# Kernel tuning notes

Measured on AMD Instinct MI355X. Metric: run time of the kernel, lower is better.

Reference implementation:

```python
import jax, jax.numpy as jnp
import numpy as np
import math

DIM = 1024
DIM_HEAD = 64
HEADS = 16
B, N = 2, 2048


def _layernorm(x, g, b, eps=1e-5):
    x32 = x.astype(jnp.float32)
    mu = jnp.mean(x32, axis=-1, keepdims=True)
    var = jnp.var(x32, axis=-1, keepdims=True)
    return ((x32 - mu) * jax.lax.rsqrt(var + eps) * g + b).astype(x.dtype)


def setup_inputs() -> dict:
    key = jax.random.key(0)
    ks = jax.random.split(key, 8)
    inner = DIM_HEAD * HEADS
    return {
        "x": jax.random.normal(ks[0], (B, N, DIM), dtype=jnp.float32),
        "w_q": jax.random.normal(ks[1], (inner, DIM), dtype=jnp.float32) * 0.02,
        "w_kv": jax.random.normal(ks[2], (2 * DIM_HEAD, DIM), dtype=jnp.float32) * 0.02,
        "w_out": jax.random.normal(ks[3], (DIM, inner), dtype=jnp.float32) * 0.02,
        "ln_g": jnp.ones((DIM,), dtype=jnp.float32),
        "ln_b": jnp.zeros((DIM,), dtype=jnp.float32),
        "lno_g": jnp.ones((DIM,), dtype=jnp.float32),
        "lno_b": jnp.zeros((DIM,), dtype=jnp.float32),
    }


def reference(x, w_q, w_kv, w_out, ln_g, ln_b, lno_g, lno_b):
    b, n, _ = x.shape
    scale = DIM_HEAD ** -0.5
    xn = _layernorm(x, ln_g, ln_b)
    q = jnp.einsum('bnc,ec->bne', xn, w_q)                 # [b, n, h*d]
    kv = jnp.einsum('bnc,ec->bne', xn, w_kv)               # [b, n, 2*d]
    k, v = jnp.split(kv, 2, axis=-1)                        # each [b, n, d]
    q = q.reshape(b, n, HEADS, DIM_HEAD).transpose(0, 2, 1, 3)  # [b, h, n, d]
    # faithful double scaling: q*scale then q,k each *sqrt(scale)
    sqs = math.sqrt(scale)
    q = q * (scale * sqs)
    k = k * sqs
    sim = jnp.einsum('bhid,bjd->bhij', q, k)                # [b, h, n, n]
    max_neg = -jnp.finfo(sim.dtype).max
    causal_mask = jnp.triu(jnp.ones((n, n), dtype=bool), k=1)
    sim = jnp.where(causal_mask, max_neg, sim)
    attn = jax.nn.softmax(sim.astype(jnp.float32), axis=-1).astype(sim.dtype)
    out = jnp.einsum('bhij,bjd->bhid', attn, v)             # [b, h, n, d]
    out = out.transpose(0, 2, 1, 3).reshape(b, n, HEADS * DIM_HEAD)
    out = jnp.einsum('bne,ce->bnc', out, w_out)             # [b, n, dim]
    return _layernorm(out, lno_g, lno_b)
```

## Files before the change

### kernel.cpp

```cpp
#include <hip/hip_runtime.h>
#include <hip/hip_bf16.h>
#include <stdint.h>

typedef unsigned short u16;
typedef __bf16 bf16x8 __attribute__((ext_vector_type(8)));
typedef float f32x4 __attribute__((ext_vector_type(4)));

#define MFMA16(a, b, c) __builtin_amdgcn_mfma_f32_16x16x32_bf16((a), (b), (c), 0, 0, 0)

#define BATCH 2
#define NSEQ 2048
#define DIMC 1024
#define NHEAD 16
#define DHEAD 64

__device__ __forceinline__ u16 f2bf(float f) {
  unsigned u = __float_as_uint(f);
  u += 0x7FFFu + ((u >> 16) & 1u);
  return (u16)(u >> 16);
}
__device__ __forceinline__ float bf2f(u16 h) {
  return __uint_as_float(((unsigned)h) << 16);
}
__device__ __forceinline__ void gload_lds16(const void* g, void* lds) {
  __builtin_amdgcn_global_load_lds((const __attribute__((address_space(1))) void*)g,
                                   (__attribute__((address_space(3))) void*)lds,
                                   16, 0, 0);
}
#define WAIT_VM(N) asm volatile("s_waitcnt vmcnt(" #N ")" ::: "memory")
#define BARRIER() __builtin_amdgcn_s_barrier()

__global__ __launch_bounds__(256) void cvt_f32_bf16(const float* __restrict__ in,
                                                    u16* __restrict__ out, int n) {
  int i = (blockIdx.x * 256 + threadIdx.x) * 4;
  if (i < n) {
    float4 v = *(const float4*)(in + i);
    ushort4 o;
    o.x = f2bf(v.x); o.y = f2bf(v.y); o.z = f2bf(v.z); o.w = f2bf(v.w);
    *(ushort4*)(out + i) = o;
  }
}

__global__ __launch_bounds__(256) void ln_f32_to_bf16(const float* __restrict__ X,
                                                      const float* __restrict__ G,
                                                      const float* __restrict__ Bv,
                                                      u16* __restrict__ Y) {
  const int row = blockIdx.x;
  const int tid = threadIdx.x;
  const float4 v = *(const float4*)(X + (size_t)row * DIMC + tid * 4);
  float s = v.x + v.y + v.z + v.w;
  float q = v.x * v.x + v.y * v.y + v.z * v.z + v.w * v.w;
#pragma unroll
  for (int d = 1; d < 64; d <<= 1) {
    s += __shfl_xor(s, d, 64);
    q += __shfl_xor(q, d, 64);
  }
  __shared__ float ps[4], pq[4];
  const int w = tid >> 6, l = tid & 63;
  if (l == 0) { ps[w] = s; pq[w] = q; }
  __syncthreads();
  s = ps[0] + ps[1] + ps[2] + ps[3];
  q = pq[0] + pq[1] + pq[2] + pq[3];
  const float mean = s * (1.f / DIMC);
  const float var = q * (1.f / DIMC) - mean * mean;
  const float rs = rsqrtf(var + 1e-5f);
  const float4 g = *(const float4*)(G + tid * 4);
  const float4 bb = *(const float4*)(Bv + tid * 4);
  ushort4 o;
  o.x = f2bf((v.x - mean) * rs * g.x + bb.x);
  o.y = f2bf((v.y - mean) * rs * g.y + bb.y);
  o.z = f2bf((v.z - mean) * rs * g.z + bb.z);
  o.w = f2bf((v.w - mean) * rs * g.w + bb.w);
  *(ushort4*)(Y + (size_t)row * DIMC + tid * 4) = o;
}

__global__ __launch_bounds__(256) void ln_bf16_to_f32(const u16* __restrict__ X,
                                                      const float* __restrict__ G,
                                                      const float* __restrict__ Bv,
                                                      float* __restrict__ Y) {
  const int row = blockIdx.x;
  const int tid = threadIdx.x;
  const ushort4 hv = *(const ushort4*)(X + (size_t)row * DIMC + tid * 4);
  float x0 = bf2f(hv.x), x1 = bf2f(hv.y), x2 = bf2f(hv.z), x3 = bf2f(hv.w);
  float s = x0 + x1 + x2 + x3;
  float q = x0 * x0 + x1 * x1 + x2 * x2 + x3 * x3;
#pragma unroll
  for (int d = 1; d < 64; d <<= 1) {
    s += __shfl_xor(s, d, 64);
    q += __shfl_xor(q, d, 64);
  }
  __shared__ float ps[4], pq[4];
  const int w = tid >> 6, l = tid & 63;
  if (l == 0) { ps[w] = s; pq[w] = q; }
  __syncthreads();
  s = ps[0] + ps[1] + ps[2] + ps[3];
  q = pq[0] + pq[1] + pq[2] + pq[3];
  const float mean = s * (1.f / DIMC);
  const float var = q * (1.f / DIMC) - mean * mean;
  const float rs = rsqrtf(var + 1e-5f);
  const float4 g = *(const float4*)(G + tid * 4);
  const float4 bb = *(const float4*)(Bv + tid * 4);
  float4 o;
  o.x = (x0 - mean) * rs * g.x + bb.x;
  o.y = (x1 - mean) * rs * g.y + bb.y;
  o.z = (x2 - mean) * rs * g.z + bb.z;
  o.w = (x3 - mean) * rs * g.w + bb.w;
  *(float4*)(Y + (size_t)row * DIMC + tid * 4) = o;
}

template <int MODE>
__global__ __launch_bounds__(512, 4) void gemm_bt(const u16* __restrict__ A,
                                                  const u16* __restrict__ Bw,
                                                  u16* __restrict__ out0,
                                                  u16* __restrict__ out1,
                                                  u16* __restrict__ out2,
                                                  int M, int N, int K, float scale0) {
  const int tid = threadIdx.x;
  const int w = tid >> 6, l = tid & 63;
  const int wr = w >> 2, wc = w & 3;
  const int lr = l & 15, lg = l >> 4;

  const int nwgx = gridDim.x;
  const int nwg = nwgx * gridDim.y;
  int flat = blockIdx.x + nwgx * blockIdx.y;
  flat = (flat & 7) * (nwg >> 3) + (flat >> 3);
  const int m0 = (flat / nwgx) * 128, n0 = (flat % nwgx) * 128;

  __shared__ u16 As[2][128 * 64];
  __shared__ u16 Bs[2][128 * 64];

  f32x4 acc[4][2] = {};

  auto STAGE = [&](int buf, int kt) {
#pragma unroll
    for (int r = 0; r < 2; ++r) {
      const int c = w * 2 + r;
      const int lo = c * 1024 + l * 16;
      const int row = lo >> 7;
      const int cl = (lo & 127) ^ ((row & 7) << 4);
      gload_lds16((const char*)A + ((size_t)(m0 + row) * K + kt * 64) * 2 + cl,
                  (char*)As[buf] + c * 1024);
      gload_lds16((const char*)Bw + ((size_t)(n0 + row) * K + kt * 64) * 2 + cl,
                  (char*)Bs[buf] + c * 1024);
    }
  };

  const int nk = K >> 6;
  STAGE(0, 0);
  STAGE(1, 1);
  int cur = 0;
  for (int kt = 0; kt < nk; ++kt) {
    if (kt + 1 < nk) { WAIT_VM(4); } else { WAIT_VM(0); }
    BARRIER();
    const char* as = (const char*)As[cur];
    const char* bs = (const char*)Bs[cur];
#pragma unroll
    for (int ks = 0; ks < 2; ++ks) {
      bf16x8 af[4], bfr[2];
#pragma unroll
      for (int mi = 0; mi < 4; ++mi) {
        const int row = wr * 64 + mi * 16 + lr;
        af[mi] = *(const bf16x8*)(as + row * 128 + ((ks * 64 + lg * 16) ^ ((row & 7) << 4)));
      }
#pragma unroll
      for (int ni = 0; ni < 2; ++ni) {
        const int row = wc * 32 + ni * 16 + lr;
        bfr[ni] = *(const bf16x8*)(bs + row * 128 + ((ks * 64 + lg * 16) ^ ((row & 7) << 4)));
      }
      __builtin_amdgcn_s_setprio(1);
#pragma unroll
      for (int mi = 0; mi < 4; ++mi)
#pragma unroll
        for (int ni = 0; ni < 2; ++ni)
          acc[mi][ni] = MFMA16(af[mi], bfr[ni], acc[mi][ni]);
      __builtin_amdgcn_s_setprio(0);
    }
    BARRIER();
    if (kt + 2 < nk) STAGE(cur, kt + 2);
    cur ^= 1;
  }

  if constexpr (MODE == 0) {
#pragma unroll
    for (int mi = 0; mi < 4; ++mi)
#pragma unroll
      for (int ni = 0; ni < 2; ++ni)
#pragma unroll
        for (int r = 0; r < 4; ++r) {
          const int row = m0 + wr * 64 + mi * 16 + lg * 4 + r;
          const int col = n0 + wc * 32 + ni * 16 + lr;
          out0[(size_t)row * N + col] = f2bf(acc[mi][ni][r] * scale0);
        }
  } else {
    const float sqs = 0.35355339059327379f;
#pragma unroll
    for (int mi = 0; mi < 4; ++mi)
#pragma unroll
      for (int ni = 0; ni < 2; ++ni)
#pragma unroll
        for (int r = 0; r < 4; ++r) {
          const int m = m0 + wr * 64 + mi * 16 + lg * 4 + r;
          const int col = n0 + wc * 32 + ni * 16 + lr;
          const float vv = acc[mi][ni][r];
          if (col < 1024) {
            out0[(size_t)m * 1024 + col] = f2bf(vv * scale0);
          } else {
            const int b = m >> 11, n = m & 2047;
            const int colk = col - 1024;
            if (colk < 64) {
              out1[(size_t)m * 64 + colk] = f2bf(vv * sqs);
            } else {
              const int d = colk - 64;
              out2[((size_t)b * 64 + d) * NSEQ + n] = f2bf(vv);
            }
          }
        }
  }
}

__global__ __launch_bounds__(256) void attn_causal(const u16* __restrict__ Q,
                                                   const u16* __restrict__ Kg,
                                                   const u16* __restrict__ VTg,
                                                   u16* __restrict__ O) {
  const int pi = blockIdx.x;
  const int qtA = pi, qtB = 31 - pi;
  const int bh = blockIdx.y;
  const int b = bh >> 4, h = bh & 15;
  const int tid = threadIdx.x;
  const int w = tid >> 6, l = tid & 63;
  const int lr = l & 15, lg = l >> 4;

  __shared__ u16 Ks[2][64 * 64];
  __shared__ u16 Vs[2][64 * 64];
  __shared__ u16 Ps[4][16 * 64];

  const int qrowA = qtA * 64 + w * 16 + lr;
  const int qrowB = qtB * 64 + w * 16 + lr;
  const size_t qbA = ((size_t)(b * NSEQ + qrowA)) * DIMC + h * DHEAD;
  const size_t qbB = ((size_t)(b * NSEQ + qrowB)) * DIMC + h * DHEAD;
  const bf16x8 aqA0 = *(const bf16x8*)(Q + qbA + lg * 8);
  const bf16x8 aqA1 = *(const bf16x8*)(Q + qbA + 32 + lg * 8);
  const bf16x8 aqB0 = *(const bf16x8*)(Q + qbB + lg * 8);
  const bf16x8 aqB1 = *(const bf16x8*)(Q + qbB + 32 + lg * 8);

  const char* kb = (const char*)(Kg + (size_t)b * NSEQ * DHEAD);
  const char* vb = (const char*)(VTg + (size_t)b * DHEAD * NSEQ);

  float mA[4], lA[4], mB[4], lB[4];
  f32x4 oA[4], oB[4];
#pragma unroll
  for (int r = 0; r < 4; ++r) { mA[r] = -1e30f; lA[r] = 0.f; mB[r] = -1e30f; lB[r] = 0.f; }
#pragma unroll
  for (int f = 0; f < 4; ++f) { oA[f] = f32x4{0.f,0.f,0.f,0.f}; oB[f] = f32x4{0.f,0.f,0.f,0.f}; }

  auto STAGE = [&](int buf, int kt) {
#pragma unroll
    for (int r = 0; r < 2; ++r) {
      const int c = w * 2 + r;
      const int lo = c * 1024 + l * 16;
      const int row = lo >> 7;
      const int cl = (lo & 127) ^ ((row & 7) << 4);
      gload_lds16(kb + (size_t)(kt * 64 + row) * 128 + cl, (char*)Ks[buf] + c * 1024);
      gload_lds16(vb + (size_t)row * (NSEQ * 2) + kt * 128 + cl, (char*)Vs[buf] + c * 1024);
    }
  };

  auto TILE = [&](const bf16x8 q0, const bf16x8 q1, float* mr, float* lsum,
                  f32x4* oa, int qt, int kt, int cur) {
    f32x4 s[4];
    __builtin_amdgcn_s_setprio(1);
#pragma unroll
    for (int f = 0; f < 4; ++f) {
      s[f] = f32x4{0.f, 0.f, 0.f, 0.f};
      const int krow = f * 16 + lr;
      const char* krp = (const char*)Ks[cur] + krow * 128;
      const int ksw = (krow & 7) << 4;
      const bf16x8 b0 = *(const bf16x8*)(krp + ((lg * 16) ^ ksw));
      const bf16x8 b1 = *(const bf16x8*)(krp + ((64 + lg * 16) ^ ksw));
      s[f] = MFMA16(q0, b0, s[f]);
      s[f] = MFMA16(q1, b1, s[f]);
    }
    __builtin_amdgcn_s_setprio(0);

    if (kt == qt) {
#pragma unroll
      for (int f = 0; f < 4; ++f)
#pragma unroll
        for (int r = 0; r < 4; ++r)
          if (f * 16 + lr > w * 16 + lg * 4 + r) s[f][r] = -1e30f;
    }

    float mx[4];
#pragma unroll
    for (int r = 0; r < 4; ++r) {
      float v = fmaxf(fmaxf(s[0][r], s[1][r]), fmaxf(s[2][r], s[3][r]));
#pragma unroll
      for (int d = 1; d < 16; d <<= 1) v = fmaxf(v, __shfl_xor(v, d, 64));
      mx[r] = v;
    }
    const bool grow = (mx[0] - mr[0] > 6.f) || (mx[1] - mr[1] > 6.f) ||
                      (mx[2] - mr[2] > 6.f) || (mx[3] - mr[3] > 6.f);
    if (__any(grow)) {
#pragma unroll
      for (int r = 0; r < 4; ++r) {
        const float mnew = fmaxf(mr[r], mx[r]);
        const float sc = exp2f(mr[r] - mnew);
        lsum[r] *= sc;
        mr[r] = mnew;
#pragma unroll
        for (int f = 0; f < 4; ++f) oa[f][r] *= sc;
      }
    }
#pragma unroll
    for (int r = 0; r < 4; ++r) {
      float ls = 0.f;
#pragma unroll
      for (int f = 0; f < 4; ++f) {
        const float p = exp2f(s[f][r] - mr[r]);
        s[f][r] = p;
        ls += p;
      }
#pragma unroll
      for (int d = 1; d < 16; d <<= 1) ls += __shfl_xor(ls, d, 64);
      lsum[r] += ls;
    }

    u16* pw = &Ps[w][0];
#pragma unroll
    for (int f = 0; f < 4; ++f)
#pragma unroll
      for (int r = 0; r < 4; ++r) {
        const int row = lg * 4 + r;
        const int cbyte = (f * 16 + lr) * 2;
        *(u16*)((char*)pw + row * 128 + (cbyte ^ ((row & 7) << 4))) =
            (u16)(__float_as_uint(s[f][r]) >> 16);
      }

    const int psw = (lr & 7) << 4;
    const bf16x8 ap0 = *(const bf16x8*)((const char*)pw + lr * 128 + ((lg * 16) ^ psw));
    const bf16x8 ap1 = *(const bf16x8*)((const char*)pw + lr * 128 + ((64 + lg * 16) ^ psw));
    __builtin_amdgcn_s_setprio(1);
#pragma unroll
    for (int f = 0; f < 4; ++f) {
      const int vrow = f * 16 + lr;
      const char* vr = (const char*)Vs[cur] + vrow * 128;
      const int vsw = (vrow & 7) << 4;
      const bf16x8 b0 = *(const bf16x8*)(vr + ((lg * 16) ^ vsw));
      const bf16x8 b1 = *(const bf16x8*)(vr + ((64 + lg * 16) ^ vsw));
      oa[f] = MFMA16(ap0, b0, oa[f]);
      oa[f] = MFMA16(ap1, b1, oa[f]);
    }
    __builtin_amdgcn_s_setprio(0);
  };

  const int nkt = qtB + 1;
  STAGE(0, 0);
  __syncthreads();
  int cur = 0;
  for (int kt = 0; kt < nkt; ++kt) {
    if (kt + 1 < nkt) STAGE(cur ^ 1, kt + 1);
    if (kt <= qtA) TILE(aqA0, aqA1, mA, lA, oA, qtA, kt, cur);
    TILE(aqB0, aqB1, mB, lB, oB, qtB, kt, cur);
    __syncthreads();
    cur ^= 1;
  }

  float invA[4], invB[4];
#pragma unroll
  for (int r = 0; r < 4; ++r) { invA[r] = 1.f / lA[r]; invB[r] = 1.f / lB[r]; }
#pragma unroll
  for (int f = 0; f < 4; ++f)
#pragma unroll
    for (int r = 0; r < 4; ++r) {
      const int col = h * DHEAD + f * 16 + lr;
      const int rowA = qtA * 64 + w * 16 + lg * 4 + r;
      O[((size_t)(b * NSEQ + rowA)) * DIMC + col] = f2bf(oA[f][r] * invA[r]);
      const int rowB = qtB * 64 + w * 16 + lg * 4 + r;
      O[((size_t)(b * NSEQ + rowB)) * DIMC + col] = f2bf(oB[f][r] * invB[r]);
    }
}

extern "C" void kernel_launch(void* const* d_in, const int* in_sizes, int n_in,
                              void* d_out, int out_size, void* d_ws, size_t ws_size,
                              hipStream_t stream) {
  const float* x = (const float*)d_in[0];
  const float* w_q = (const float*)d_in[1];
  const float* w_kv = (const float*)d_in[2];
  const float* w_out = (const float*)d_in[3];
  const float* ln_g = (const float*)d_in[4];
  const float* ln_b = (const float*)d_in[5];
  const float* lno_g = (const float*)d_in[6];
  const float* lno_b = (const float*)d_in[7];
  float* out = (float*)d_out;

  char* ws = (char*)d_ws;
  size_t off = 0;
  auto alloc = [&](size_t bytes) {
    char* p = ws + off;
    off += (bytes + 255) & ~(size_t)255;
    return p;
  };
  u16* xn    = (u16*)alloc((size_t)BATCH * NSEQ * DIMC * 2);
  u16* wqkv  = (u16*)alloc((size_t)1152 * DIMC * 2);
  u16* wob   = (u16*)alloc((size_t)DIMC * DIMC * 2);
  u16* qb    = (u16*)alloc((size_t)BATCH * NSEQ * DIMC * 2);
  u16* kb    = (u16*)alloc((size_t)BATCH * NSEQ * DHEAD * 2);
  u16* vtb   = (u16*)alloc((size_t)BATCH * DHEAD * NSEQ * 2);
  u16* ao = xn;
  u16* yb = qb;

  const float qscale = (float)(0.044194173824159216 * 1.4426950408889634);

  cvt_f32_bf16<<<1024, 256, 0, stream>>>(w_q, wqkv, DIMC * DIMC);
  cvt_f32_bf16<<<128, 256, 0, stream>>>(w_kv, wqkv + (size_t)DIMC * DIMC, 128 * DIMC);
  cvt_f32_bf16<<<1024, 256, 0, stream>>>(w_out, wob, DIMC * DIMC);

  ln_f32_to_bf16<<<BATCH * NSEQ, 256, 0, stream>>>(x, ln_g, ln_b, xn);

  gemm_bt<2><<<dim3(9, 32), 512, 0, stream>>>(xn, wqkv, qb, kb, vtb,
                                              BATCH * NSEQ, 1152, DIMC, qscale);

  attn_causal<<<dim3(16, 32), 256, 0, stream>>>(qb, kb, vtb, ao);

  gemm_bt<0><<<dim3(8, 32), 512, 0, stream>>>(ao, wob, yb, nullptr, nullptr,
                                              BATCH * NSEQ, DIMC, DIMC, 1.f);

  ln_bf16_to_f32<<<BATCH * NSEQ, 256, 0, stream>>>(yb, lno_g, lno_b, out);
}
```

Baseline: 211.4 us.

## Shrink GEMM tile to 64x128 with 4 waves; drop lazy softmax rescale in attention

The GEMM kernel now uses 64x128 output tiles with 256 threads (4 waves each owning 64x32) instead of 128x128 with 512 threads. The grid doubles along M to give more workgroups for better CU occupancy, at the cost of lower arithmetic intensity per tile. The staging loop and the wait counts are adjusted to match the new load split. The attention kernel also replaces the conditional lazy rescale (applied only when the row max grew by more than 6) with an unconditional per-row online-softmax rescale, which adds exp and multiply work on every tile.

```diff
diff --git a/kernel.cpp b/kernel.cpp
--- a/kernel.cpp
+++ b/kernel.cpp
@@ -109,24 +109,23 @@
 }
 
 template <int MODE>
-__global__ __launch_bounds__(512, 4) void gemm_bt(const u16* __restrict__ A,
-                                                  const u16* __restrict__ Bw,
-                                                  u16* __restrict__ out0,
-                                                  u16* __restrict__ out1,
-                                                  u16* __restrict__ out2,
-                                                  int M, int N, int K, float scale0) {
+__global__ __launch_bounds__(256) void gemm_bt(const u16* __restrict__ A,
+                                               const u16* __restrict__ Bw,
+                                               u16* __restrict__ out0,
+                                               u16* __restrict__ out1,
+                                               u16* __restrict__ out2,
+                                               int M, int N, int K, float scale0) {
   const int tid = threadIdx.x;
   const int w = tid >> 6, l = tid & 63;
-  const int wr = w >> 2, wc = w & 3;
   const int lr = l & 15, lg = l >> 4;
 
   const int nwgx = gridDim.x;
   const int nwg = nwgx * gridDim.y;
   int flat = blockIdx.x + nwgx * blockIdx.y;
   flat = (flat & 7) * (nwg >> 3) + (flat >> 3);
-  const int m0 = (flat / nwgx) * 128, n0 = (flat % nwgx) * 128;
-
-  __shared__ u16 As[2][128 * 64];
+  const int m0 = (flat / nwgx) * 64, n0 = (flat % nwgx) * 128;
+
+  __shared__ u16 As[2][64 * 64];
   __shared__ u16 Bs[2][128 * 64];
 
   f32x4 acc[4][2] = {};
@@ -140,6 +139,13 @@
       const int cl = (lo & 127) ^ ((row & 7) << 4);
       gload_lds16((const char*)A + ((size_t)(m0 + row) * K + kt * 64) * 2 + cl,
                   (char*)As[buf] + c * 1024);
+    }
+#pragma unroll
+    for (int r = 0; r < 4; ++r) {
+      const int c = w * 4 + r;
+      const int lo = c * 1024 + l * 16;
+      const int row = lo >> 7;
+      const int cl = (lo & 127) ^ ((row & 7) << 4);
       gload_lds16((const char*)Bw + ((size_t)(n0 + row) * K + kt * 64) * 2 + cl,
                   (char*)Bs[buf] + c * 1024);
     }
@@ -150,7 +156,7 @@
   STAGE(1, 1);
   int cur = 0;
   for (int kt = 0; kt < nk; ++kt) {
-    if (kt + 1 < nk) { WAIT_VM(4); } else { WAIT_VM(0); }
+    if (kt + 1 < nk) { WAIT_VM(6); } else { WAIT_VM(0); }
     BARRIER();
     const char* as = (const char*)As[cur];
     const char* bs = (const char*)Bs[cur];
@@ -159,12 +165,12 @@
       bf16x8 af[4], bfr[2];
 #pragma unroll
       for (int mi = 0; mi < 4; ++mi) {
-        const int row = wr * 64 + mi * 16 + lr;
+        const int row = mi * 16 + lr;
         af[mi] = *(const bf16x8*)(as + row * 128 + ((ks * 64 + lg * 16) ^ ((row & 7) << 4)));
       }
 #pragma unroll
       for (int ni = 0; ni < 2; ++ni) {
-        const int row = wc * 32 + ni * 16 + lr;
+        const int row = w * 32 + ni * 16 + lr;
         bfr[ni] = *(const bf16x8*)(bs + row * 128 + ((ks * 64 + lg * 16) ^ ((row & 7) << 4)));
       }
       __builtin_amdgcn_s_setprio(1);
@@ -187,8 +193,8 @@
       for (int ni = 0; ni < 2; ++ni)
 #pragma unroll
         for (int r = 0; r < 4; ++r) {
-          const int row = m0 + wr * 64 + mi * 16 + lg * 4 + r;
-          const int col = n0 + wc * 32 + ni * 16 + lr;
+          const int row = m0 + mi * 16 + lg * 4 + r;
+          const int col = n0 + w * 32 + ni * 16 + lr;
           out0[(size_t)row * N + col] = f2bf(acc[mi][ni][r] * scale0);
         }
   } else {
@@ -199,8 +205,8 @@
       for (int ni = 0; ni < 2; ++ni)
 #pragma unroll
         for (int r = 0; r < 4; ++r) {
-          const int m = m0 + wr * 64 + mi * 16 + lg * 4 + r;
-          const int col = n0 + wc * 32 + ni * 16 + lr;
+          const int m = m0 + mi * 16 + lg * 4 + r;
+          const int col = n0 + w * 32 + ni * 16 + lr;
           const float vv = acc[mi][ni][r];
           if (col < 1024) {
             out0[(size_t)m * 1024 + col] = f2bf(vv * scale0);
@@ -290,39 +296,26 @@
           if (f * 16 + lr > w * 16 + lg * 4 + r) s[f][r] = -1e30f;
     }
 
-    float mx[4];
 #pragma unroll
     for (int r = 0; r < 4; ++r) {
-      float v = fmaxf(fmaxf(s[0][r], s[1][r]), fmaxf(s[2][r], s[3][r]));
-#pragma unroll
-      for (int d = 1; d < 16; d <<= 1) v = fmaxf(v, __shfl_xor(v, d, 64));
-      mx[r] = v;
-    }
-    const bool grow = (mx[0] - mr[0] > 6.f) || (mx[1] - mr[1] > 6.f) ||
-                      (mx[2] - mr[2] > 6.f) || (mx[3] - mr[3] > 6.f);
-    if (__any(grow)) {
-#pragma unroll
-      for (int r = 0; r < 4; ++r) {
-        const float mnew = fmaxf(mr[r], mx[r]);
-        const float sc = exp2f(mr[r] - mnew);
-        lsum[r] *= sc;
-        mr[r] = mnew;
-#pragma unroll
-        for (int f = 0; f < 4; ++f) oa[f][r] *= sc;
-      }
-    }
-#pragma unroll
-    for (int r = 0; r < 4; ++r) {
+      float mx = fmaxf(fmaxf(s[0][r], s[1][r]), fmaxf(s[2][r], s[3][r]));
+#pragma unroll
+      for (int d = 1; d < 16; d <<= 1) mx = fmaxf(mx, __shfl_xor(mx, d, 64));
+      const float mnew = fmaxf(mr[r], mx);
+      const float sc = exp2f(mr[r] - mnew);
       float ls = 0.f;
 #pragma unroll
       for (int f = 0; f < 4; ++f) {
-        const float p = exp2f(s[f][r] - mr[r]);
+        const float p = exp2f(s[f][r] - mnew);
         s[f][r] = p;
         ls += p;
       }
 #pragma unroll
       for (int d = 1; d < 16; d <<= 1) ls += __shfl_xor(ls, d, 64);
-      lsum[r] += ls;
+      lsum[r] = lsum[r] * sc + ls;
+      mr[r] = mnew;
+#pragma unroll
+      for (int f = 0; f < 4; ++f) oa[f][r] *= sc;
     }
 
     u16* pw = &Ps[w][0];
@@ -417,12 +410,12 @@
 
   ln_f32_to_bf16<<<BATCH * NSEQ, 256, 0, stream>>>(x, ln_g, ln_b, xn);
 
-  gemm_bt<2><<<dim3(9, 32), 512, 0, stream>>>(xn, wqkv, qb, kb, vtb,
+  gemm_bt<2><<<dim3(9, 64), 256, 0, stream>>>(xn, wqkv, qb, kb, vtb,
                                               BATCH * NSEQ, 1152, DIMC, qscale);
 
   attn_causal<<<dim3(16, 32), 256, 0, stream>>>(qb, kb, vtb, ao);
 
-  gemm_bt<0><<<dim3(8, 32), 512, 0, stream>>>(ao, wob, yb, nullptr, nullptr,
+  gemm_bt<0><<<dim3(8, 64), 256, 0, stream>>>(ao, wob, yb, nullptr, nullptr,
                                               BATCH * NSEQ, DIMC, DIMC, 1.f);
 
   ln_bf16_to_f32<<<BATCH * NSEQ, 256, 0, stream>>>(yb, lno_g, lno_b, out);
```

Result: faster. 203.8 us (-3.6%).

## Make attention waves independent with direct global K/V loads and per-wave row pairing

Applied to the files above, without the earlier changes.

Rewrites the causal attention kernel so each wave independently handles two 16-row query chunks (c and 127-c), loading K and V fragments straight from global memory instead of staging them in shared memory with block-wide barriers. The lazy rescale threshold is dropped, so every tile rescales. This removes __syncthreads and LDS staging and gives finer causal load balance. In exchange, K/V reuse across the waves of a block is lost, which raises global and L2 traffic. The gemm launch bound's minimum occupancy hint is also removed.

```diff
diff --git a/kernel.cpp b/kernel.cpp
--- a/kernel.cpp
+++ b/kernel.cpp
@@ -109,12 +109,12 @@
 }
 
 template <int MODE>
-__global__ __launch_bounds__(512, 4) void gemm_bt(const u16* __restrict__ A,
-                                                  const u16* __restrict__ Bw,
-                                                  u16* __restrict__ out0,
-                                                  u16* __restrict__ out1,
-                                                  u16* __restrict__ out2,
-                                                  int M, int N, int K, float scale0) {
+__global__ __launch_bounds__(512) void gemm_bt(const u16* __restrict__ A,
+                                               const u16* __restrict__ Bw,
+                                               u16* __restrict__ out0,
+                                               u16* __restrict__ out1,
+                                               u16* __restrict__ out2,
+                                               int M, int N, int K, float scale0) {
   const int tid = threadIdx.x;
   const int w = tid >> 6, l = tid & 63;
   const int wr = w >> 2, wc = w & 3;
@@ -222,162 +222,118 @@
                                                    const u16* __restrict__ Kg,
                                                    const u16* __restrict__ VTg,
                                                    u16* __restrict__ O) {
-  const int pi = blockIdx.x;
-  const int qtA = pi, qtB = 31 - pi;
-  const int bh = blockIdx.y;
-  const int b = bh >> 4, h = bh & 15;
   const int tid = threadIdx.x;
   const int w = tid >> 6, l = tid & 63;
   const int lr = l & 15, lg = l >> 4;
-
-  __shared__ u16 Ks[2][64 * 64];
-  __shared__ u16 Vs[2][64 * 64];
+  const int gw = blockIdx.x * 4 + w;
+  const int bh = gw & 31;
+  const int b = bh >> 4, h = bh & 15;
+  const int p = gw >> 5;
+
   __shared__ u16 Ps[4][16 * 64];
-
-  const int qrowA = qtA * 64 + w * 16 + lr;
-  const int qrowB = qtB * 64 + w * 16 + lr;
-  const size_t qbA = ((size_t)(b * NSEQ + qrowA)) * DIMC + h * DHEAD;
-  const size_t qbB = ((size_t)(b * NSEQ + qrowB)) * DIMC + h * DHEAD;
-  const bf16x8 aqA0 = *(const bf16x8*)(Q + qbA + lg * 8);
-  const bf16x8 aqA1 = *(const bf16x8*)(Q + qbA + 32 + lg * 8);
-  const bf16x8 aqB0 = *(const bf16x8*)(Q + qbB + lg * 8);
-  const bf16x8 aqB1 = *(const bf16x8*)(Q + qbB + 32 + lg * 8);
+  u16* pw = &Ps[w][0];
 
   const char* kb = (const char*)(Kg + (size_t)b * NSEQ * DHEAD);
   const char* vb = (const char*)(VTg + (size_t)b * DHEAD * NSEQ);
 
-  float mA[4], lA[4], mB[4], lB[4];
-  f32x4 oA[4], oB[4];
-#pragma unroll
-  for (int r = 0; r < 4; ++r) { mA[r] = -1e30f; lA[r] = 0.f; mB[r] = -1e30f; lB[r] = 0.f; }
-#pragma unroll
-  for (int f = 0; f < 4; ++f) { oA[f] = f32x4{0.f,0.f,0.f,0.f}; oB[f] = f32x4{0.f,0.f,0.f,0.f}; }
-
-  auto STAGE = [&](int buf, int kt) {
-#pragma unroll
-    for (int r = 0; r < 2; ++r) {
-      const int c = w * 2 + r;
-      const int lo = c * 1024 + l * 16;
-      const int row = lo >> 7;
-      const int cl = (lo & 127) ^ ((row & 7) << 4);
-      gload_lds16(kb + (size_t)(kt * 64 + row) * 128 + cl, (char*)Ks[buf] + c * 1024);
-      gload_lds16(vb + (size_t)row * (NSEQ * 2) + kt * 128 + cl, (char*)Vs[buf] + c * 1024);
+  const f32x4 ZERO4 = {0.f, 0.f, 0.f, 0.f};
+
+#pragma unroll
+  for (int half = 0; half < 2; ++half) {
+    const int c = half ? (127 - p) : p;
+    const int qrow = c * 16 + lr;
+    const size_t qbase = ((size_t)(b * NSEQ + qrow)) * DIMC + h * DHEAD;
+    const bf16x8 q0 = *(const bf16x8*)(Q + qbase + lg * 8);
+    const bf16x8 q1 = *(const bf16x8*)(Q + qbase + 32 + lg * 8);
+
+    float mr[4], lsum[4];
+    f32x4 oa[4];
+#pragma unroll
+    for (int r = 0; r < 4; ++r) { mr[r] = -1e30f; lsum[r] = 0.f; }
+#pragma unroll
+    for (int f = 0; f < 4; ++f) oa[f] = ZERO4;
+
+    const int dt = c >> 2;
+    for (int kt = 0; kt <= dt; ++kt) {
+      f32x4 s[4];
+      __builtin_amdgcn_s_setprio(1);
+#pragma unroll
+      for (int f = 0; f < 4; ++f) {
+        const char* kr = kb + (size_t)(kt * 64 + f * 16 + lr) * 128;
+        const bf16x8 kf0 = *(const bf16x8*)(kr + lg * 16);
+        const bf16x8 kf1 = *(const bf16x8*)(kr + 64 + lg * 16);
+        s[f] = MFMA16(q0, kf0, ZERO4);
+        s[f] = MFMA16(q1, kf1, s[f]);
+      }
+      __builtin_amdgcn_s_setprio(0);
+
+      if (kt == dt) {
+#pragma unroll
+        for (int f = 0; f < 4; ++f)
+#pragma unroll
+          for (int r = 0; r < 4; ++r)
+            if (kt * 64 + f * 16 + lr > c * 16 + lg * 4 + r) s[f][r] = -1e30f;
+      }
+
+#pragma unroll
+      for (int r = 0; r < 4; ++r) {
+        float mx = fmaxf(fmaxf(s[0][r], s[1][r]), fmaxf(s[2][r], s[3][r]));
+#pragma unroll
+        for (int d = 1; d < 16; d <<= 1) mx = fmaxf(mx, __shfl_xor(mx, d, 64));
+        const float mnew = fmaxf(mr[r], mx);
+        const float sc = exp2f(mr[r] - mnew);
+        float ls = 0.f;
+#pragma unroll
+        for (int f = 0; f < 4; ++f) {
+          const float pv = exp2f(s[f][r] - mnew);
+          s[f][r] = pv;
+          ls += pv;
+        }
+#pragma unroll
+        for (int d = 1; d < 16; d <<= 1) ls += __shfl_xor(ls, d, 64);
+        lsum[r] = lsum[r] * sc + ls;
+        mr[r] = mnew;
+#pragma unroll
+        for (int f = 0; f < 4; ++f) oa[f][r] *= sc;
+      }
+
+#pragma unroll
+      for (int f = 0; f < 4; ++f)
+#pragma unroll
+        for (int r = 0; r < 4; ++r) {
+          const int row = lg * 4 + r;
+          const int cbyte = (f * 16 + lr) * 2;
+          *(u16*)((char*)pw + row * 128 + (cbyte ^ ((row & 7) << 4))) =
+              (u16)(__float_as_uint(s[f][r]) >> 16);
+        }
+
+      const int psw = (lr & 7) << 4;
+      const bf16x8 ap0 = *(const bf16x8*)((const char*)pw + lr * 128 + ((lg * 16) ^ psw));
+      const bf16x8 ap1 = *(const bf16x8*)((const char*)pw + lr * 128 + ((64 + lg * 16) ^ psw));
+      __builtin_amdgcn_s_setprio(1);
+#pragma unroll
+      for (int f = 0; f < 4; ++f) {
+        const char* vr = vb + (size_t)(f * 16 + lr) * (NSEQ * 2) + kt * 128;
+        const bf16x8 vf0 = *(const bf16x8*)(vr + lg * 16);
+        const bf16x8 vf1 = *(const bf16x8*)(vr + 64 + lg * 16);
+        oa[f] = MFMA16(ap0, vf0, oa[f]);
+        oa[f] = MFMA16(ap1, vf1, oa[f]);
+      }
+      __builtin_amdgcn_s_setprio(0);
     }
-  };
-
-  auto TILE = [&](const bf16x8 q0, const bf16x8 q1, float* mr, float* lsum,
-                  f32x4* oa, int qt, int kt, int cur) {
-    f32x4 s[4];
-    __builtin_amdgcn_s_setprio(1);
-#pragma unroll
-    for (int f = 0; f < 4; ++f) {
-      s[f] = f32x4{0.f, 0.f, 0.f, 0.f};
-      const int krow = f * 16 + lr;
-      const char* krp = (const char*)Ks[cur] + krow * 128;
-      const int ksw = (krow & 7) << 4;
-      const bf16x8 b0 = *(const bf16x8*)(krp + ((lg * 16) ^ ksw));
-      const bf16x8 b1 = *(const bf16x8*)(krp + ((64 + lg * 16) ^ ksw));
-      s[f] = MFMA16(q0, b0, s[f]);
-      s[f] = MFMA16(q1, b1, s[f]);
-    }
-    __builtin_amdgcn_s_setprio(0);
-
-    if (kt == qt) {
-#pragma unroll
-      for (int f = 0; f < 4; ++f)
-#pragma unroll
-        for (int r = 0; r < 4; ++r)
-          if (f * 16 + lr > w * 16 + lg * 4 + r) s[f][r] = -1e30f;
-    }
-
-    float mx[4];
-#pragma unroll
-    for (int r = 0; r < 4; ++r) {
-      float v = fmaxf(fmaxf(s[0][r], s[1][r]), fmaxf(s[2][r], s[3][r]));
-#pragma unroll
-      for (int d = 1; d < 16; d <<= 1) v = fmaxf(v, __shfl_xor(v, d, 64));
-      mx[r] = v;
-    }
-    const bool grow = (mx[0] - mr[0] > 6.f) || (mx[1] - mr[1] > 6.f) ||
-                      (mx[2] - mr[2] > 6.f) || (mx[3] - mr[3] > 6.f);
-    if (__any(grow)) {
+
+    float inv[4];
+#pragma unroll
+    for (int r = 0; r < 4; ++r) inv[r] = 1.f / lsum[r];
+#pragma unroll
+    for (int f = 0; f < 4; ++f)
 #pragma unroll
       for (int r = 0; r < 4; ++r) {
-        const float mnew = fmaxf(mr[r], mx[r]);
-        const float sc = exp2f(mr[r] - mnew);
-        lsum[r] *= sc;
-        mr[r] = mnew;
-#pragma unroll
-        for (int f = 0; f < 4; ++f) oa[f][r] *= sc;
-      }
-    }
-#pragma unroll
-    for (int r = 0; r < 4; ++r) {
-      float ls = 0.f;
-#pragma unroll
-      for (int f = 0; f < 4; ++f) {
-        const float p = exp2f(s[f][r] - mr[r]);
-        s[f][r] = p;
-        ls += p;
-      }
-#pragma unroll
-      for (int d = 1; d < 16; d <<= 1) ls += __shfl_xor(ls, d, 64);
-      lsum[r] += ls;
-    }
-
-    u16* pw = &Ps[w][0];
-#pragma unroll
-    for (int f = 0; f < 4; ++f)
-#pragma unroll
-      for (int r = 0; r < 4; ++r) {
-        const int row = lg * 4 + r;
-        const int cbyte = (f * 16 + lr) * 2;
-        *(u16*)((char*)pw + row * 128 + (cbyte ^ ((row & 7) << 4))) =
-            (u16)(__float_as_uint(s[f][r]) >> 16);
-      }
-
-    const int psw = (lr & 7) << 4;
-    const bf16x8 ap0 = *(const bf16x8*)((const char*)pw + lr * 128 + ((lg * 16) ^ psw));
-    const bf16x8 ap1 = *(const bf16x8*)((const char*)pw + lr * 128 + ((64 + lg * 16) ^ psw));
-    __builtin_amdgcn_s_setprio(1);
-#pragma unroll
-    for (int f = 0; f < 4; ++f) {
-      const int vrow = f * 16 + lr;
-      const char* vr = (const char*)Vs[cur] + vrow * 128;
-      const int vsw = (vrow & 7) << 4;
-      const bf16x8 b0 = *(const bf16x8*)(vr + ((lg * 16) ^ vsw));
-      const bf16x8 b1 = *(const bf16x8*)(vr + ((64 + lg * 16) ^ vsw));
-      oa[f] = MFMA16(ap0, b0, oa[f]);
-      oa[f] = MFMA16(ap1, b1, oa[f]);
-    }
-    __builtin_amdgcn_s_setprio(0);
-  };
-
-  const int nkt = qtB + 1;
-  STAGE(0, 0);
-  __syncthreads();
-  int cur = 0;
-  for (int kt = 0; kt < nkt; ++kt) {
-    if (kt + 1 < nkt) STAGE(cur ^ 1, kt + 1);
-    if (kt <= qtA) TILE(aqA0, aqA1, mA, lA, oA, qtA, kt, cur);
-    TILE(aqB0, aqB1, mB, lB, oB, qtB, kt, cur);
-    __syncthreads();
-    cur ^= 1;
-  }
-
-  float invA[4], invB[4];
-#pragma unroll
-  for (int r = 0; r < 4; ++r) { invA[r] = 1.f / lA[r]; invB[r] = 1.f / lB[r]; }
-#pragma unroll
-  for (int f = 0; f < 4; ++f)
-#pragma unroll
-    for (int r = 0; r < 4; ++r) {
-      const int col = h * DHEAD + f * 16 + lr;
-      const int rowA = qtA * 64 + w * 16 + lg * 4 + r;
-      O[((size_t)(b * NSEQ + rowA)) * DIMC + col] = f2bf(oA[f][r] * invA[r]);
-      const int rowB = qtB * 64 + w * 16 + lg * 4 + r;
-      O[((size_t)(b * NSEQ + rowB)) * DIMC + col] = f2bf(oB[f][r] * invB[r]);
-    }
+        const int row = c * 16 + lg * 4 + r;
+        const int col = h * DHEAD + f * 16 + lr;
+        O[((size_t)(b * NSEQ + row)) * DIMC + col] = f2bf(oa[f][r] * inv[r]);
+      }
+  }
 }
 
 extern "C" void kernel_launch(void* const* d_in, const int* in_sizes, int n_in,
@@ -420,7 +376,7 @@
   gemm_bt<2><<<dim3(9, 32), 512, 0, stream>>>(xn, wqkv, qb, kb, vtb,
                                               BATCH * NSEQ, 1152, DIMC, qscale);
 
-  attn_causal<<<dim3(16, 32), 256, 0, stream>>>(qb, kb, vtb, ao);
+  attn_causal<<<512, 256, 0, stream>>>(qb, kb, vtb, ao);
 
   gemm_bt<0><<<dim3(8, 32), 512, 0, stream>>>(ao, wob, yb, nullptr, nullptr,
                                               BATCH * NSEQ, DIMC, DIMC, 1.f);
```

Result: slower. 259.5 us (+22.8%).
